# Kernel tuning notes

Measured on AMD Instinct MI355X. Metric: run time of the kernel, lower is better.

Reference implementation:

```python
import jax, jax.numpy as jnp
import numpy as np

N_NODES = 50000
N_EDGES = 800000
IN_DIM = 64
OUT_DIM = 64
N_REL = 8
N_RULES = 32
N_ACTIVE = 4
LN_EPS = 1e-5


def _seg_softmax(scores, seg, num_segments):
    # numerically stable softmax within each destination segment
    m = jax.ops.segment_max(scores, seg, num_segments=num_segments)
    e = jnp.exp(scores - m[seg])
    d = jax.ops.segment_sum(e, seg, num_segments=num_segments)
    return e / d[seg]


def setup_inputs() -> dict:
    key = jax.random.key(0)
    ks = jax.random.split(key, 12)
    x = jax.random.normal(ks[0], (N_NODES, IN_DIM), dtype=jnp.float32)
    edge_index = jax.random.randint(ks[1], (2, N_EDGES), 0, N_NODES, dtype=jnp.int64)
    edge_type = jax.random.randint(ks[2], (N_EDGES,), 0, N_REL, dtype=jnp.int64)
    rule_ids = jax.random.randint(ks[3], (N_ACTIVE,), 0, N_RULES, dtype=jnp.int64)
    # parameters (xavier-ish scales)
    W_r = jax.random.normal(ks[4], (N_REL, IN_DIM, OUT_DIM), dtype=jnp.float32) * (2.0 / (IN_DIM + OUT_DIM)) ** 0.5
    Wq_w = jax.random.normal(ks[5], (IN_DIM, OUT_DIM), dtype=jnp.float32) * (1.0 / IN_DIM) ** 0.5
    Wq_bias = jnp.zeros((OUT_DIM,), dtype=jnp.float32)
    Wk_w = jax.random.normal(ks[6], (3 * IN_DIM, OUT_DIM), dtype=jnp.float32) * (1.0 / (3 * IN_DIM)) ** 0.5
    Wk_bias = jnp.zeros((OUT_DIM,), dtype=jnp.float32)
    rule_emb = jax.random.normal(ks[7], (N_RULES, IN_DIM), dtype=jnp.float32) * (2.0 / (N_RULES + IN_DIM)) ** 0.5
    bias = jnp.zeros((OUT_DIM,), dtype=jnp.float32)
    ln_g = jnp.ones((OUT_DIM,), dtype=jnp.float32)
    ln_b = jnp.zeros((OUT_DIM,), dtype=jnp.float32)
    return {"x": x, "edge_index": edge_index, "edge_type": edge_type, "rule_ids": rule_ids,
            "W_r": W_r, "Wq_w": Wq_w, "Wq_bias": Wq_bias, "Wk_w": Wk_w, "Wk_bias": Wk_bias,
            "rule_emb": rule_emb, "bias": bias, "ln_g": ln_g, "ln_b": ln_b}


def reference(x, edge_index, edge_type, rule_ids, W_r, Wq_w, Wq_bias, Wk_w, Wk_bias,
              rule_emb, bias, ln_g, ln_b):
    src, dst = edge_index[0], edge_index[1]
    num_nodes, in_dim = x.shape
    num_rel, _, out_dim = W_r.shape
    x_src = x[src]                                  # [E, in]

    # query (rule-independent): W_q(x[dst])
    q = x[dst] @ Wq_w + Wq_bias                     # [E, out]

    # relation embedding per edge: mean over output dim of W_r
    rel_emb = W_r.mean(axis=-1)[edge_type]          # [E, in]

    # split W_k over the concat [x_src, rel_emb, rule_emb]
    Wk1, Wk2, Wk3 = Wk_w[:in_dim], Wk_w[in_dim:2 * in_dim], Wk_w[2 * in_dim:]
    key_base = x_src @ Wk1 + rel_emb @ Wk2 + Wk_bias  # [E, out]
    h_R = rule_emb[rule_ids]                        # [nR, in]
    key_rule = h_R @ Wk3                            # [nR, out]

    scale = 1.0 / (out_dim ** 0.5)
    score_base = jnp.einsum('eo,eo->e', q, key_base)      # [E]
    score_rule = jnp.einsum('eo,ro->er', q, key_rule)     # [E, nR]
    scores = (score_base[:, None] + score_rule) * scale   # [E, nR]

    # per-rule scatter_softmax over destination nodes
    attn = jax.vmap(lambda s: _seg_softmax(s, dst, num_nodes),
                    in_axes=1, out_axes=1)(scores)         # [E, nR]
    mean_attn = attn.mean(axis=1)                          # [E] (combined/num_rules)

    # per-relation message: x[src] @ W_r[edge_type] (rule-independent)
    msg = jnp.zeros((x_src.shape[0], out_dim), dtype=x.dtype)
    for r in range(num_rel):
        msg = jnp.where((edge_type == r)[:, None], x_src @ W_r[r], msg)

    out = jax.ops.segment_sum(msg * mean_attn[:, None], dst, num_segments=num_nodes)
    out = out + bias
    mu = out.mean(axis=-1, keepdims=True)
    var = ((out - mu) ** 2).mean(axis=-1, keepdims=True)
    out = (out - mu) * jax.lax.rsqrt(var + LN_EPS) * ln_g + ln_b
    return jax.nn.relu(out)  # dropout is identity in eval mode
```

## Files before the change

### kernel.cpp

```cpp
#include <hip/hip_runtime.h>
#include <hip/hip_bf16.h>

#define NDIM 64
#define NREL 8
#define SCALE 0.125f
#define LN_EPS 1e-5f
#define SRC_MASK 0x07FFFFFF

typedef __bf16 bf16x8v __attribute__((ext_vector_type(8)));
typedef float f32x4v __attribute__((ext_vector_type(4)));

__device__ __forceinline__ float wave_sum64(float v) {
#pragma unroll
  for (int off = 32; off > 0; off >>= 1) v += __shfl_xor(v, off, 64);
  return v;
}
__device__ __forceinline__ float wave_max64(float v) {
#pragma unroll
  for (int off = 32; off > 0; off >>= 1) v = fmaxf(v, __shfl_xor(v, off, 64));
  return v;
}
__device__ __forceinline__ unsigned short f2bf_u(float f) {
  __hip_bfloat16 h = __float2bfloat16(f);
  return *reinterpret_cast<unsigned short*>(&h);
}
__device__ __forceinline__ float bfu2f(unsigned short u) {
  return __uint_as_float(((unsigned)u) << 16);
}
__device__ __forceinline__ float rdl_f(float v, int i) {
  return __int_as_float(__builtin_amdgcn_readlane(__float_as_int(v), i));
}

__global__ void k0_fused(const float* __restrict__ W_r,
                         const float* __restrict__ Wk_w,
                         __hip_bfloat16* __restrict__ Whi,
                         __hip_bfloat16* __restrict__ Wlo,
                         float* __restrict__ relkey) {
  int tid = threadIdx.x;
  if (blockIdx.x < 128) {
    int idx = blockIdx.x * 256 + tid;
    int j = idx & 7;
    int l = (idx >> 3) & 63;
    int ks = (idx >> 9) & 15;
    int ct = idx >> 13;
    int k = ks * 32 + (l >> 4) * 8 + j;
    int col = ct * 16 + (l & 15);
    float v = W_r[(size_t)k * 64 + col];
    __hip_bfloat16 h = __float2bfloat16(v);
    Whi[idx] = h;
    Wlo[idx] = __float2bfloat16(v - __bfloat162float(h));
    return;
  }
  __shared__ float relemb[NREL * NDIM];
  for (int idx = tid; idx < NREL * NDIM; idx += 256) {
    int r = idx >> 6, i = idx & 63;
    const float* wr = W_r + (size_t)(r * NDIM + i) * NDIM;
    float s = 0.f;
#pragma unroll
    for (int o = 0; o < NDIM; ++o) s += wr[o];
    relemb[idx] = s * (1.0f / NDIM);
  }
  __syncthreads();
  for (int idx = tid; idx < NREL * NDIM; idx += 256) {
    int r = idx >> 6, o = idx & 63;
    float s = 0.f;
#pragma unroll
    for (int i = 0; i < NDIM; ++i) s += relemb[r * NDIM + i] * Wk_w[(NDIM + i) * NDIM + o];
    relkey[idx] = s;
  }
}

__global__ void k1c_xbf(const float* __restrict__ x, __hip_bfloat16* __restrict__ xbf,
                        int total4) {
  int i = blockIdx.x * blockDim.x + threadIdx.x;
  int stride = gridDim.x * blockDim.x;
  for (; i < total4; i += stride) {
    float4 v = *reinterpret_cast<const float4*>(x + (size_t)i * 4);
    ushort4 u;
    u.x = f2bf_u(v.x); u.y = f2bf_u(v.y); u.z = f2bf_u(v.z); u.w = f2bf_u(v.w);
    *reinterpret_cast<ushort4*>(reinterpret_cast<unsigned short*>(xbf) +
                                (size_t)i * 4) = u;
  }
}

__global__ void k1_qkb(const float* __restrict__ x,
                       const float* __restrict__ Wq_w,
                       const float* __restrict__ Wq_bias,
                       const float* __restrict__ Wk_w,
                       const float* __restrict__ relkey,
                       float* __restrict__ Q, __hip_bfloat16* __restrict__ KBbf,
                       float* __restrict__ QR, int n_nodes) {
  __shared__ float xs[64][68];
  __shared__ float ws[64][128];
  __shared__ float rks[NREL][NDIM];
  int tid = threadIdx.x;
  int n0 = blockIdx.x * 64;
  for (int idx = tid; idx < 64 * 128; idx += 256) {
    int r = idx >> 7, c = idx & 127;
    ws[r][c] = (c < 64) ? Wq_w[r * 64 + c] : Wk_w[r * 64 + (c - 64)];
  }
  for (int idx = tid; idx < NREL * NDIM; idx += 256)
    rks[idx >> 6][idx & 63] = relkey[idx];
  for (int idx = tid; idx < 64 * 16; idx += 256) {
    int r = idx >> 4, c4 = (idx & 15) * 4;
    int n = n0 + r;
    float4 v = make_float4(0.f, 0.f, 0.f, 0.f);
    if (n < n_nodes) v = *reinterpret_cast<const float4*>(x + (size_t)n * 64 + c4);
    *reinterpret_cast<float4*>(&xs[r][c4]) = v;
  }
  __syncthreads();
  int tx = tid & 15, ty = tid >> 4;
  float acc[4][8] = {};
  for (int k = 0; k < 64; k += 4) {
    float4 a[4];
#pragma unroll
    for (int i = 0; i < 4; ++i) a[i] = *reinterpret_cast<float4*>(&xs[ty * 4 + i][k]);
#pragma unroll
    for (int kk = 0; kk < 4; ++kk) {
      float4 w0 = *reinterpret_cast<float4*>(&ws[k + kk][tx * 8]);
      float4 w1 = *reinterpret_cast<float4*>(&ws[k + kk][tx * 8 + 4]);
#pragma unroll
      for (int i = 0; i < 4; ++i) {
        float av = (kk == 0) ? a[i].x : (kk == 1) ? a[i].y : (kk == 2) ? a[i].z : a[i].w;
        acc[i][0] += av * w0.x; acc[i][1] += av * w0.y;
        acc[i][2] += av * w0.z; acc[i][3] += av * w0.w;
        acc[i][4] += av * w1.x; acc[i][5] += av * w1.y;
        acc[i][6] += av * w1.z; acc[i][7] += av * w1.w;
      }
    }
  }
  float qv[4][8];
#pragma unroll
  for (int i = 0; i < 4; ++i) {
    int n = n0 + ty * 4 + i;
    bool nv = n < n_nodes;
#pragma unroll
    for (int j = 0; j < 8; ++j) {
      int c = tx * 8 + j;
      if (c < 64) {
        qv[i][j] = acc[i][j] + Wq_bias[c];
        if (nv) Q[(size_t)n * 64 + c] = qv[i][j];
      } else {
        qv[i][j] = 0.f;
      }
    }
    if (nv && tx >= 8) {
      ushort4 u0, u1;
      u0.x = f2bf_u(acc[i][0]); u0.y = f2bf_u(acc[i][1]);
      u0.z = f2bf_u(acc[i][2]); u0.w = f2bf_u(acc[i][3]);
      u1.x = f2bf_u(acc[i][4]); u1.y = f2bf_u(acc[i][5]);
      u1.z = f2bf_u(acc[i][6]); u1.w = f2bf_u(acc[i][7]);
      unsigned short* kp = reinterpret_cast<unsigned short*>(KBbf) +
                           ((size_t)n << 6) + (tx - 8) * 8;
      *reinterpret_cast<ushort4*>(kp) = u0;
      *reinterpret_cast<ushort4*>(kp + 4) = u1;
    }
  }
#pragma unroll
  for (int r = 0; r < NREL; ++r) {
    float rk8[8];
    *reinterpret_cast<float4*>(&rk8[0]) =
        *reinterpret_cast<float4*>(&rks[r][(tx & 7) * 8]);
    *reinterpret_cast<float4*>(&rk8[4]) =
        *reinterpret_cast<float4*>(&rks[r][(tx & 7) * 8 + 4]);
#pragma unroll
    for (int i = 0; i < 4; ++i) {
      float pq = 0.f;
#pragma unroll
      for (int j = 0; j < 8; ++j) pq += qv[i][j] * rk8[j];
      pq += __shfl_xor(pq, 1, 64);
      pq += __shfl_xor(pq, 2, 64);
      pq += __shfl_xor(pq, 4, 64);
      pq += __shfl_xor(pq, 8, 64);
      int n = n0 + ty * 4 + i;
      if (tx == r && n < n_nodes) QR[(size_t)n * NREL + r] = pq;
    }
  }
}

__global__ void k2_hist(const int* __restrict__ dst, int* __restrict__ counts,
                        int* __restrict__ rank, int E) {
  int e = blockIdx.x * blockDim.x + threadIdx.x;
  if (e < E) rank[e] = atomicAdd(&counts[dst[e]], 1);
}

__global__ void scan_a(const int* __restrict__ counts, int* __restrict__ partial,
                       int* __restrict__ blocksums, int n) {
  __shared__ int wsum[4];
  int tid = threadIdx.x, lane = tid & 63, wv = tid >> 6;
  int base = blockIdx.x * 1024 + tid * 4;
  int4 v = make_int4(0, 0, 0, 0);
  if (base + 3 < n) v = *reinterpret_cast<const int4*>(counts + base);
  else {
    if (base < n) v.x = counts[base];
    if (base + 1 < n) v.y = counts[base + 1];
    if (base + 2 < n) v.z = counts[base + 2];
  }
  int tsum = v.x + v.y + v.z + v.w;
  int s = tsum;
#pragma unroll
  for (int off = 1; off < 64; off <<= 1) {
    int y = __shfl_up(s, off, 64);
    if (lane >= off) s += y;
  }
  if (lane == 63) wsum[wv] = s;
  __syncthreads();
  int woff = 0;
  for (int w = 0; w < wv; ++w) woff += wsum[w];
  int o0 = woff + s - tsum;
  if (base < n) partial[base] = o0;
  if (base + 1 < n) partial[base + 1] = o0 + v.x;
  if (base + 2 < n) partial[base + 2] = o0 + v.x + v.y;
  if (base + 3 < n) partial[base + 3] = o0 + v.x + v.y + v.z;
  if (tid == 255) blocksums[blockIdx.x] = woff + s;
}

__global__ void scan_b(const int* __restrict__ blocksums, int* __restrict__ blockoff,
                       int nb, int* __restrict__ offsets, int n) {
  int lane = threadIdx.x;
  int v = (lane < nb) ? blocksums[lane] : 0;
  int s = v;
#pragma unroll
  for (int off = 1; off < 64; off <<= 1) {
    int y = __shfl_up(s, off, 64);
    if (lane >= off) s += y;
  }
  if (lane < nb) blockoff[lane] = s - v;
  if (lane == 63) offsets[n] = s;
}

__global__ void scan_c(const int* __restrict__ partial, const int* __restrict__ blockoff,
                       int* __restrict__ offsets, int n) {
  int i = blockIdx.x * 256 + threadIdx.x;
  if (i < n) offsets[i] = partial[i] + blockoff[i >> 10];
}

__global__ void k2_scatter(const int* __restrict__ dst, const int* __restrict__ src,
                           const int* __restrict__ et, const int* __restrict__ rank,
                           const int* __restrict__ offsets,
                           int2* __restrict__ ed2, int E) {
  int e = blockIdx.x * blockDim.x + threadIdx.x;
  if (e < E) {
    int d = dst[e];
    int p = offsets[d] + rank[e];
    ed2[p] = make_int2(src[e] | (et[e] << 27), d);
  }
}

__global__ void k3_scores(const float* __restrict__ Q,
                          const __hip_bfloat16* __restrict__ KBbf,
                          const float* __restrict__ QR,
                          const int2* __restrict__ ed2,
                          float* __restrict__ scores, int E) {
  int tid = threadIdx.x;
  int lane = tid & 63;
  int li = lane & 15, sub = lane >> 4, wv = tid >> 6;
  int pos_base = blockIdx.x * 16 + wv * 4;
  int pos = pos_base + sub;
  int pc = min(pos, E - 1);
  int2 ed = ed2[pc];
  int sn = ed.x & SRC_MASK, r = (unsigned)ed.x >> 27;
  int dn = ed.y;
  float4 q = *reinterpret_cast<const float4*>(Q + (size_t)dn * 64 + li * 4);
  ushort4 u = *reinterpret_cast<const ushort4*>(
      reinterpret_cast<const unsigned short*>(KBbf) + ((size_t)sn << 6) + li * 4);
  float p = q.x * bfu2f(u.x) + q.y * bfu2f(u.y) + q.z * bfu2f(u.z) + q.w * bfu2f(u.w);
#pragma unroll
  for (int off = 1; off < 16; off <<= 1) p += __shfl_xor(p, off, 64);
  float sc = (p + QR[(size_t)dn * NREL + r]) * SCALE;
  float sg = __shfl(sc, (lane & 3) * 16, 64);
  if (lane < 4 && pos_base + lane < E) scores[pos_base + lane] = sg;
}

#define ACC_SWITCH(rr, v)                    \
  switch (rr) {                              \
    case 0: acc[0] += (v); break;            \
    case 1: acc[1] += (v); break;            \
    case 2: acc[2] += (v); break;            \
    case 3: acc[3] += (v); break;            \
    case 4: acc[4] += (v); break;            \
    case 5: acc[5] += (v); break;            \
    case 6: acc[6] += (v); break;            \
    case 7: acc[7] += (v); break;            \
  }

__global__ void k4_agg(const __hip_bfloat16* __restrict__ xb,
                       const float* __restrict__ scores,
                       const int* __restrict__ offsets,
                       const int2* __restrict__ ed2,
                       __hip_bfloat16* __restrict__ A, int n_nodes) {
  int lane = threadIdx.x & 63, wv = threadIdx.x >> 6;
  int n = blockIdx.x * 4 + wv;
  if (n >= n_nodes) return;
  const unsigned short* xbp = reinterpret_cast<const unsigned short*>(xb);
  int s0 = offsets[n], s1 = offsets[n + 1];
  int deg = s1 - s0;
  float acc[8] = {0.f, 0.f, 0.f, 0.f, 0.f, 0.f, 0.f, 0.f};
  if (deg > 0 && deg <= 64) {
    int p = s0 + lane;
    bool valid = p < s1;
    float sc = valid ? scores[p] : -1e30f;
    int se = valid ? ed2[p].x : 0;
    float m = wave_max64(sc);
    float ex = valid ? __expf(sc - m) : 0.f;
    float t = wave_sum64(ex);
    float wl = ex * (1.0f / t);
    int i = 0;
    for (; i + 4 <= deg; i += 4) {
      float w0 = rdl_f(wl, i), w1 = rdl_f(wl, i + 1);
      float w2 = rdl_f(wl, i + 2), w3 = rdl_f(wl, i + 3);
      int se0 = __builtin_amdgcn_readlane(se, i);
      int se1 = __builtin_amdgcn_readlane(se, i + 1);
      int se2 = __builtin_amdgcn_readlane(se, i + 2);
      int se3 = __builtin_amdgcn_readlane(se, i + 3);
      unsigned short u0 = xbp[((size_t)(se0 & SRC_MASK) << 6) + lane];
      unsigned short u1 = xbp[((size_t)(se1 & SRC_MASK) << 6) + lane];
      unsigned short u2 = xbp[((size_t)(se2 & SRC_MASK) << 6) + lane];
      unsigned short u3 = xbp[((size_t)(se3 & SRC_MASK) << 6) + lane];
      float v0 = w0 * bfu2f(u0);
      float v1 = w1 * bfu2f(u1);
      float v2 = w2 * bfu2f(u2);
      float v3 = w3 * bfu2f(u3);
      int r0 = (unsigned)se0 >> 27, r1 = (unsigned)se1 >> 27;
      int r2 = (unsigned)se2 >> 27, r3 = (unsigned)se3 >> 27;
      ACC_SWITCH(r0, v0)
      ACC_SWITCH(r1, v1)
      ACC_SWITCH(r2, v2)
      ACC_SWITCH(r3, v3)
    }
    for (; i < deg; ++i) {
      float wgt = rdl_f(wl, i);
      int sei = __builtin_amdgcn_readlane(se, i);
      float v = wgt * bfu2f(xbp[((size_t)(sei & SRC_MASK) << 6) + lane]);
      int rr = (unsigned)sei >> 27;
      ACC_SWITCH(rr, v)
    }
  } else if (deg > 64) {
    float m = -1e30f;
    for (int c = s0; c < s1; c += 64) {
      int p = c + lane;
      float s = (p < s1) ? scores[p] : -1e30f;
      m = fmaxf(m, s);
    }
    m = wave_max64(m);
    float t = 0.f;
    for (int c = s0; c < s1; c += 64) {
      int p = c + lane;
      t += (p < s1) ? __expf(scores[p] - m) : 0.f;
    }
    t = wave_sum64(t);
    float inv = 1.0f / t;
    for (int c = s0; c < s1; c += 64) {
      int p = c + lane;
      bool valid = p < s1;
      int se = valid ? ed2[p].x : 0;
      float wl = valid ? __expf(scores[p] - m) * inv : 0.f;
      int cnt = min(64, s1 - c);
      for (int i = 0; i < cnt; ++i) {
        float wgt = rdl_f(wl, i);
        int sei = __builtin_amdgcn_readlane(se, i);
        float v = wgt * bfu2f(xbp[((size_t)(sei & SRC_MASK) << 6) + lane]);
        int rr = (unsigned)sei >> 27;
        ACC_SWITCH(rr, v)
      }
    }
  }
#pragma unroll
  for (int r = 0; r < 8; ++r)
    A[(size_t)n * 512 + r * 64 + lane] = __float2bfloat16(acc[r]);
}

__global__ void __launch_bounds__(256) k5_mfma_ln(
    const __hip_bfloat16* __restrict__ A,
    const __hip_bfloat16* __restrict__ Whi,
    const __hip_bfloat16* __restrict__ Wlo,
    const float* __restrict__ bias,
    const float* __restrict__ ln_g, const float* __restrict__ ln_b,
    float* __restrict__ out, int n_nodes) {
  int tid = threadIdx.x;
  int lane = tid & 63, w = tid >> 6;
  int li = lane & 15, gr = lane >> 4;
  int n0 = blockIdx.x * 64;
  int arow_n = n0 + w * 16 + li;
  bool rvalid = arow_n < n_nodes;
  const __hip_bfloat16* arow = A + (size_t)arow_n * 512 + gr * 8;
  const bf16x8v* wh = reinterpret_cast<const bf16x8v*>(Whi);
  const bf16x8v* wl = reinterpret_cast<const bf16x8v*>(Wlo);
  f32x4v acc[4];
#pragma unroll
  for (int ct = 0; ct < 4; ++ct) acc[ct] = (f32x4v){0.f, 0.f, 0.f, 0.f};
  for (int ks = 0; ks < 16; ++ks) {
    uint4 au = make_uint4(0u, 0u, 0u, 0u);
    if (rvalid) au = *reinterpret_cast<const uint4*>(arow + ks * 32);
    bf16x8v a = __builtin_bit_cast(bf16x8v, au);
#pragma unroll
    for (int ct = 0; ct < 4; ++ct) {
      bf16x8v bh = wh[(ct * 16 + ks) * 64 + lane];
      bf16x8v bl = wl[(ct * 16 + ks) * 64 + lane];
      acc[ct] = __builtin_amdgcn_mfma_f32_16x16x32_bf16(a, bh, acc[ct], 0, 0, 0);
      acc[ct] = __builtin_amdgcn_mfma_f32_16x16x32_bf16(a, bl, acc[ct], 0, 0, 0);
    }
  }
  float bi[4], g[4], bb[4];
#pragma unroll
  for (int ct = 0; ct < 4; ++ct) {
    int col = ct * 16 + li;
    bi[ct] = bias[col];
    g[ct] = ln_g[col];
    bb[ct] = ln_b[col];
  }
#pragma unroll
  for (int reg = 0; reg < 4; ++reg) {
    float v[4];
#pragma unroll
    for (int ct = 0; ct < 4; ++ct) v[ct] = acc[ct][reg] + bi[ct];
    float s = v[0] + v[1] + v[2] + v[3];
    s += __shfl_xor(s, 1, 64);
    s += __shfl_xor(s, 2, 64);
    s += __shfl_xor(s, 4, 64);
    s += __shfl_xor(s, 8, 64);
    float mu = s * (1.0f / 64.0f);
    float sq = 0.f;
#pragma unroll
    for (int ct = 0; ct < 4; ++ct) {
      float d = v[ct] - mu;
      sq += d * d;
    }
    sq += __shfl_xor(sq, 1, 64);
    sq += __shfl_xor(sq, 2, 64);
    sq += __shfl_xor(sq, 4, 64);
    sq += __shfl_xor(sq, 8, 64);
    float inv = rsqrtf(sq * (1.0f / 64.0f) + LN_EPS);
    int n = n0 + w * 16 + gr * 4 + reg;
    if (n < n_nodes) {
#pragma unroll
      for (int ct = 0; ct < 4; ++ct) {
        float y = (v[ct] - mu) * inv * g[ct] + bb[ct];
        out[(size_t)n * 64 + ct * 16 + li] = fmaxf(y, 0.f);
      }
    }
  }
}

extern "C" void kernel_launch(void* const* d_in, const int* in_sizes, int n_in,
                              void* d_out, int out_size, void* d_ws, size_t ws_size,
                              hipStream_t stream) {
  (void)n_in; (void)out_size; (void)ws_size;
  const float* x = (const float*)d_in[0];
  const int* ei = (const int*)d_in[1];
  const int* et = (const int*)d_in[2];
  const float* W_r = (const float*)d_in[4];
  const float* Wq_w = (const float*)d_in[5];
  const float* Wq_b = (const float*)d_in[6];
  const float* Wk_w = (const float*)d_in[7];
  const float* bias = (const float*)d_in[10];
  const float* ln_g = (const float*)d_in[11];
  const float* ln_b = (const float*)d_in[12];

  int N = in_sizes[0] / NDIM;
  int E = in_sizes[2];
  const int* srcp = ei;
  const int* dstp = ei + E;

  char* p = (char*)d_ws;
  auto alloc = [&](size_t bytes) {
    void* r = (void*)p;
    p += (bytes + 255) & ~(size_t)255;
    return r;
  };
  float* Q = (float*)alloc((size_t)N * NDIM * 4);
  __hip_bfloat16* KBbf = (__hip_bfloat16*)alloc((size_t)N * NDIM * 2);
  float* QR = (float*)alloc((size_t)N * NREL * 4);
  float* relkey = (float*)alloc(NREL * NDIM * 4);
  __hip_bfloat16* xbf = (__hip_bfloat16*)alloc((size_t)N * NDIM * 2);
  int* counts = (int*)alloc((size_t)N * 4);
  int* partial = (int*)alloc((size_t)N * 4);
  int* offsets = (int*)alloc((size_t)(N + 1) * 4);
  int* rank = (int*)alloc((size_t)E * 4);
  int* blocksums = (int*)alloc(64 * 4);
  int* blockoff = (int*)alloc(64 * 4);
  int2* ed2 = (int2*)alloc((size_t)E * 8);
  float* scores = (float*)alloc((size_t)E * 4);
  __hip_bfloat16* A = (__hip_bfloat16*)alloc((size_t)N * (NREL * NDIM) * 2);
  __hip_bfloat16* Whi = (__hip_bfloat16*)alloc(4 * 16 * 64 * 8 * 2);
  __hip_bfloat16* Wlo = (__hip_bfloat16*)alloc(4 * 16 * 64 * 8 * 2);

  int nscan = (N + 1023) / 1024;

  hipMemsetAsync(counts, 0, (size_t)N * 4, stream);
  k0_fused<<<129, 256, 0, stream>>>(W_r, Wk_w, Whi, Wlo, relkey);
  k1c_xbf<<<1024, 256, 0, stream>>>(x, xbf, N * NDIM / 4);
  k1_qkb<<<(N + 63) / 64, 256, 0, stream>>>(x, Wq_w, Wq_b, Wk_w, relkey, Q, KBbf, QR, N);
  k2_hist<<<(E + 255) / 256, 256, 0, stream>>>(dstp, counts, rank, E);
  scan_a<<<nscan, 256, 0, stream>>>(counts, partial, blocksums, N);
  scan_b<<<1, 64, 0, stream>>>(blocksums, blockoff, nscan, offsets, N);
  scan_c<<<(N + 255) / 256, 256, 0, stream>>>(partial, blockoff, offsets, N);
  k2_scatter<<<(E + 255) / 256, 256, 0, stream>>>(dstp, srcp, et, rank, offsets, ed2, E);
  k3_scores<<<(E + 15) / 16, 256, 0, stream>>>(Q, KBbf, QR, ed2, scores, E);
  k4_agg<<<(N + 3) / 4, 256, 0, stream>>>(xbf, scores, offsets, ed2, A, N);
  k5_mfma_ln<<<(N + 63) / 64, 256, 0, stream>>>(A, Whi, Wlo, bias, ln_g, ln_b,
                                                (float*)d_out, N);
}
```

Before: 300.0 us.

## Compute node Q/K projection with split-bf16 MFMA instead of FP32 SIMT GEMM

Replaces the shared-memory FP32 register-tiled GEMM that computes per-node Q, the key base and the Q·relkey products with a matrix-core kernel. It uses 16x16x32 bf16 MFMA and a hi/lo bf16 split of both operands to keep near-FP32 accuracy. The weight split and fragment layout are precomputed in the setup kernel. The intent is to cut the ALU-bound projection time, at the cost of three MFMAs per tile and scattered 2-byte and 4-byte stores in the epilogue.

```diff
diff --git a/kernel.cpp b/kernel.cpp
--- a/kernel.cpp
+++ b/kernel.cpp
@@ -32,13 +32,17 @@
 }
 
 __global__ void k0_fused(const float* __restrict__ W_r,
+                         const float* __restrict__ Wq_w,
                          const float* __restrict__ Wk_w,
                          __hip_bfloat16* __restrict__ Whi,
                          __hip_bfloat16* __restrict__ Wlo,
+                         __hip_bfloat16* __restrict__ Wqhi,
+                         __hip_bfloat16* __restrict__ Wqlo,
                          float* __restrict__ relkey) {
   int tid = threadIdx.x;
-  if (blockIdx.x < 128) {
-    int idx = blockIdx.x * 256 + tid;
+  int b = blockIdx.x;
+  if (b < 128) {
+    int idx = b * 256 + tid;
     int j = idx & 7;
     int l = (idx >> 3) & 63;
     int ks = (idx >> 9) & 15;
@@ -51,6 +55,20 @@
     Wlo[idx] = __float2bfloat16(v - __bfloat162float(h));
     return;
   }
+  if (b < 160) {
+    int idx = (b - 128) * 256 + tid;
+    int j = idx & 7;
+    int l = (idx >> 3) & 63;
+    int ks = (idx >> 9) & 1;
+    int ct = idx >> 10;
+    int k = ks * 32 + (l >> 4) * 8 + j;
+    int col = ct * 16 + (l & 15);
+    float v = (col < 64) ? Wq_w[k * 64 + col] : Wk_w[k * 64 + (col - 64)];
+    __hip_bfloat16 h = __float2bfloat16(v);
+    Wqhi[idx] = h;
+    Wqlo[idx] = __float2bfloat16(v - __bfloat162float(h));
+    return;
+  }
   __shared__ float relemb[NREL * NDIM];
   for (int idx = tid; idx < NREL * NDIM; idx += 256) {
     int r = idx >> 6, i = idx & 63;
@@ -83,97 +101,90 @@
   }
 }
 
-__global__ void k1_qkb(const float* __restrict__ x,
-                       const float* __restrict__ Wq_w,
-                       const float* __restrict__ Wq_bias,
-                       const float* __restrict__ Wk_w,
-                       const float* __restrict__ relkey,
-                       float* __restrict__ Q, __hip_bfloat16* __restrict__ KBbf,
-                       float* __restrict__ QR, int n_nodes) {
-  __shared__ float xs[64][68];
-  __shared__ float ws[64][128];
-  __shared__ float rks[NREL][NDIM];
+__global__ void __launch_bounds__(256) k1_mfma(
+    const float* __restrict__ x,
+    const float* __restrict__ Wq_bias,
+    const __hip_bfloat16* __restrict__ Wqhi,
+    const __hip_bfloat16* __restrict__ Wqlo,
+    const float* __restrict__ relkey,
+    float* __restrict__ Q, __hip_bfloat16* __restrict__ KBbf,
+    float* __restrict__ QR, int n_nodes) {
   int tid = threadIdx.x;
+  int lane = tid & 63, w = tid >> 6;
+  int li = lane & 15, gr = lane >> 4;
   int n0 = blockIdx.x * 64;
-  for (int idx = tid; idx < 64 * 128; idx += 256) {
-    int r = idx >> 7, c = idx & 127;
-    ws[r][c] = (c < 64) ? Wq_w[r * 64 + c] : Wk_w[r * 64 + (c - 64)];
-  }
-  for (int idx = tid; idx < NREL * NDIM; idx += 256)
-    rks[idx >> 6][idx & 63] = relkey[idx];
-  for (int idx = tid; idx < 64 * 16; idx += 256) {
-    int r = idx >> 4, c4 = (idx & 15) * 4;
-    int n = n0 + r;
-    float4 v = make_float4(0.f, 0.f, 0.f, 0.f);
-    if (n < n_nodes) v = *reinterpret_cast<const float4*>(x + (size_t)n * 64 + c4);
-    *reinterpret_cast<float4*>(&xs[r][c4]) = v;
-  }
-  __syncthreads();
-  int tx = tid & 15, ty = tid >> 4;
-  float acc[4][8] = {};
-  for (int k = 0; k < 64; k += 4) {
-    float4 a[4];
-#pragma unroll
-    for (int i = 0; i < 4; ++i) a[i] = *reinterpret_cast<float4*>(&xs[ty * 4 + i][k]);
-#pragma unroll
-    for (int kk = 0; kk < 4; ++kk) {
-      float4 w0 = *reinterpret_cast<float4*>(&ws[k + kk][tx * 8]);
-      float4 w1 = *reinterpret_cast<float4*>(&ws[k + kk][tx * 8 + 4]);
-#pragma unroll
-      for (int i = 0; i < 4; ++i) {
-        float av = (kk == 0) ? a[i].x : (kk == 1) ? a[i].y : (kk == 2) ? a[i].z : a[i].w;
-        acc[i][0] += av * w0.x; acc[i][1] += av * w0.y;
-        acc[i][2] += av * w0.z; acc[i][3] += av * w0.w;
-        acc[i][4] += av * w1.x; acc[i][5] += av * w1.y;
-        acc[i][6] += av * w1.z; acc[i][7] += av * w1.w;
-      }
-    }
-  }
-  float qv[4][8];
-#pragma unroll
-  for (int i = 0; i < 4; ++i) {
-    int n = n0 + ty * 4 + i;
+  int arow = n0 + w * 16 + li;
+  bool rv = arow < n_nodes;
+  bf16x8v ahi[2], alo[2];
+#pragma unroll
+  for (int ks = 0; ks < 2; ++ks) {
+    float xv[8];
+    float4 v0 = make_float4(0.f, 0.f, 0.f, 0.f), v1 = v0;
+    if (rv) {
+      const float* xp = x + (size_t)arow * 64 + ks * 32 + gr * 8;
+      v0 = *reinterpret_cast<const float4*>(xp);
+      v1 = *reinterpret_cast<const float4*>(xp + 4);
+    }
+    xv[0] = v0.x; xv[1] = v0.y; xv[2] = v0.z; xv[3] = v0.w;
+    xv[4] = v1.x; xv[5] = v1.y; xv[6] = v1.z; xv[7] = v1.w;
+    unsigned short uh[8], ul[8];
+#pragma unroll
+    for (int j = 0; j < 8; ++j) {
+      uh[j] = f2bf_u(xv[j]);
+      ul[j] = f2bf_u(xv[j] - bfu2f(uh[j]));
+    }
+    ahi[ks] = __builtin_bit_cast(bf16x8v, *reinterpret_cast<uint4*>(uh));
+    alo[ks] = __builtin_bit_cast(bf16x8v, *reinterpret_cast<uint4*>(ul));
+  }
+  const bf16x8v* bh = reinterpret_cast<const bf16x8v*>(Wqhi);
+  const bf16x8v* bl = reinterpret_cast<const bf16x8v*>(Wqlo);
+  f32x4v acc[8];
+#pragma unroll
+  for (int ct = 0; ct < 8; ++ct) acc[ct] = (f32x4v){0.f, 0.f, 0.f, 0.f};
+#pragma unroll
+  for (int ct = 0; ct < 8; ++ct) {
+#pragma unroll
+    for (int ks = 0; ks < 2; ++ks) {
+      bf16x8v Bh = bh[(ct * 2 + ks) * 64 + lane];
+      bf16x8v Bl = bl[(ct * 2 + ks) * 64 + lane];
+      acc[ct] = __builtin_amdgcn_mfma_f32_16x16x32_bf16(ahi[ks], Bh, acc[ct], 0, 0, 0);
+      acc[ct] = __builtin_amdgcn_mfma_f32_16x16x32_bf16(ahi[ks], Bl, acc[ct], 0, 0, 0);
+      acc[ct] = __builtin_amdgcn_mfma_f32_16x16x32_bf16(alo[ks], Bh, acc[ct], 0, 0, 0);
+    }
+  }
+  float rk[NREL][4];
+#pragma unroll
+  for (int r = 0; r < NREL; ++r)
+#pragma unroll
+    for (int ct = 0; ct < 4; ++ct) rk[r][ct] = relkey[r * 64 + ct * 16 + li];
+  float bq[4];
+#pragma unroll
+  for (int ct = 0; ct < 4; ++ct) bq[ct] = Wq_bias[ct * 16 + li];
+#pragma unroll
+  for (int reg = 0; reg < 4; ++reg) {
+    int n = n0 + w * 16 + gr * 4 + reg;
     bool nv = n < n_nodes;
-#pragma unroll
-    for (int j = 0; j < 8; ++j) {
-      int c = tx * 8 + j;
-      if (c < 64) {
-        qv[i][j] = acc[i][j] + Wq_bias[c];
-        if (nv) Q[(size_t)n * 64 + c] = qv[i][j];
-      } else {
-        qv[i][j] = 0.f;
-      }
-    }
-    if (nv && tx >= 8) {
-      ushort4 u0, u1;
-      u0.x = f2bf_u(acc[i][0]); u0.y = f2bf_u(acc[i][1]);
-      u0.z = f2bf_u(acc[i][2]); u0.w = f2bf_u(acc[i][3]);
-      u1.x = f2bf_u(acc[i][4]); u1.y = f2bf_u(acc[i][5]);
-      u1.z = f2bf_u(acc[i][6]); u1.w = f2bf_u(acc[i][7]);
-      unsigned short* kp = reinterpret_cast<unsigned short*>(KBbf) +
-                           ((size_t)n << 6) + (tx - 8) * 8;
-      *reinterpret_cast<ushort4*>(kp) = u0;
-      *reinterpret_cast<ushort4*>(kp + 4) = u1;
-    }
-  }
-#pragma unroll
-  for (int r = 0; r < NREL; ++r) {
-    float rk8[8];
-    *reinterpret_cast<float4*>(&rk8[0]) =
-        *reinterpret_cast<float4*>(&rks[r][(tx & 7) * 8]);
-    *reinterpret_cast<float4*>(&rk8[4]) =
-        *reinterpret_cast<float4*>(&rks[r][(tx & 7) * 8 + 4]);
-#pragma unroll
-    for (int i = 0; i < 4; ++i) {
-      float pq = 0.f;
-#pragma unroll
-      for (int j = 0; j < 8; ++j) pq += qv[i][j] * rk8[j];
+    float qv[4];
+#pragma unroll
+    for (int ct = 0; ct < 4; ++ct) {
+      qv[ct] = acc[ct][reg] + bq[ct];
+      if (nv) Q[(size_t)n * 64 + ct * 16 + li] = qv[ct];
+    }
+    if (nv) {
+      unsigned short* kp = reinterpret_cast<unsigned short*>(KBbf) + ((size_t)n << 6);
+#pragma unroll
+      for (int ct = 4; ct < 8; ++ct)
+        kp[(ct - 4) * 16 + li] = f2bf_u(acc[ct][reg]);
+    }
+#pragma unroll
+    for (int r = 0; r < NREL; ++r) {
+      float pq = qv[0] * rk[r][0] + qv[1] * rk[r][1] +
+                 qv[2] * rk[r][2] + qv[3] * rk[r][3];
       pq += __shfl_xor(pq, 1, 64);
       pq += __shfl_xor(pq, 2, 64);
       pq += __shfl_xor(pq, 4, 64);
       pq += __shfl_xor(pq, 8, 64);
-      int n = n0 + ty * 4 + i;
-      if (tx == r && n < n_nodes) QR[(size_t)n * NREL + r] = pq;
+      if (nv && li == r) QR[(size_t)n * NREL + r] = pq;
     }
   }
 }
@@ -484,13 +495,16 @@
   __hip_bfloat16* A = (__hip_bfloat16*)alloc((size_t)N * (NREL * NDIM) * 2);
   __hip_bfloat16* Whi = (__hip_bfloat16*)alloc(4 * 16 * 64 * 8 * 2);
   __hip_bfloat16* Wlo = (__hip_bfloat16*)alloc(4 * 16 * 64 * 8 * 2);
+  __hip_bfloat16* Wqhi = (__hip_bfloat16*)alloc(8 * 2 * 64 * 8 * 2);
+  __hip_bfloat16* Wqlo = (__hip_bfloat16*)alloc(8 * 2 * 64 * 8 * 2);
 
   int nscan = (N + 1023) / 1024;
 
   hipMemsetAsync(counts, 0, (size_t)N * 4, stream);
-  k0_fused<<<129, 256, 0, stream>>>(W_r, Wk_w, Whi, Wlo, relkey);
+  k0_fused<<<161, 256, 0, stream>>>(W_r, Wq_w, Wk_w, Whi, Wlo, Wqhi, Wqlo, relkey);
   k1c_xbf<<<1024, 256, 0, stream>>>(x, xbf, N * NDIM / 4);
-  k1_qkb<<<(N + 63) / 64, 256, 0, stream>>>(x, Wq_w, Wq_b, Wk_w, relkey, Q, KBbf, QR, N);
+  k1_mfma<<<(N + 63) / 64, 256, 0, stream>>>(x, Wq_b, Wqhi, Wqlo, relkey, Q, KBbf,
+                                             QR, N);
   k2_hist<<<(E + 255) / 256, 256, 0, stream>>>(dstp, counts, rank, E);
   scan_a<<<nscan, 256, 0, stream>>>(counts, partial, blocksums, N);
   scan_b<<<1, 64, 0, stream>>>(blocksums, blockoff, nscan, offsets, N);
```

Measured after the change: 272.8 us. -9.1%, faster.
